# Kernel tuning notes

Hardware: AMD Instinct MI355X
Metric: run time of the kernel (lower is better)

Reference implementation:

```python
import jax, jax.numpy as jnp
import numpy as np
from jax.scipy.linalg import solve_triangular

B, N, C = 4, 1024, 1024
H, P = 16, 5
D = C // H
CHUNK = 64
EPS = 1e-8


def l2norm(x):
    return x * jax.lax.rsqrt(jnp.sum(x * x, -1, keepdims=True) + 1e-6)


def fir_conv(x, filt):
    # x: (B,N,H,D); filt: (H,D,K); causal depthwise FIR along sequence dim
    K = filt.shape[-1]
    n = x.shape[1]
    xp = jnp.pad(x, ((0, 0), (K - 1, 0), (0, 0), (0, 0)))
    out = jnp.zeros_like(x)
    for j in range(K):  # K in {3,7}: tiny fixed tap loop
        out = out + filt[:, :, j] * xp[:, j:j + n]
    return out


def cross_mix(x, mix):
    # residual low-magnitude cross-head mixing: (H,H) matrix applied over head axis
    return x + jnp.einsum('bnhd,hg->bngd', x, mix)


def delta_rule_chunkwise(q, k, v, beta, chunk=CHUNK):
    # q,k,v: (B,H,N,D); beta: (B,H,N). Chunkwise DeltaNet recurrence.
    b, h, n, d = q.shape
    q = l2norm(q) * (d ** -0.5)
    k = l2norm(k)
    v = v * beta[..., None]
    kb = k * beta[..., None]
    nc = n // chunk
    qc, kc, vc, kbc = (t.reshape(b, h, nc, chunk, d) for t in (q, k, v, kb))
    # (I + strict-lower(kb k^T))^{-1} applied to kb and v via triangular solve
    A = jnp.tril(jnp.einsum('bhgcd,bhged->bhgce', kbc, kc), -1)
    M = A + jnp.eye(chunk, dtype=q.dtype)
    w = solve_triangular(M, kbc, lower=True)   # (B,H,nc,chunk,D)
    u = solve_triangular(M, vc, lower=True)
    attn_loc = jnp.tril(jnp.einsum('bhgcd,bhged->bhgce', qc, kc))  # causal intra-chunk

    def step(S, xs):
        q_i, k_i, w_i, u_i, a_i = xs
        u_adj = u_i - jnp.einsum('bhcd,bhde->bhce', w_i, S)
        o_i = jnp.einsum('bhcd,bhde->bhce', q_i, S) + jnp.einsum('bhce,bhed->bhcd', a_i, u_adj)
        S = S + jnp.einsum('bhcd,bhce->bhde', k_i, u_adj)
        return S, o_i

    S0 = jnp.zeros((b, h, d, d), q.dtype)
    xs = tuple(jnp.moveaxis(t, 2, 0) for t in (qc, kc, w, u, attn_loc))
    S, o = jax.lax.scan(step, S0, xs)
    o = jnp.moveaxis(o, 0, 2).reshape(b, h, n, d)
    return o, S


def setup_inputs() -> dict:
    key = jax.random.key(0)
    ks = jax.random.split(key, 12)
    s = C ** -0.5
    inp = {}
    inp['x'] = jax.random.normal(ks[0], (B, N, C), jnp.float32)
    inp['W_qkv'] = jax.random.normal(ks[1], (C, 3 * C), jnp.float32) * s
    inp['W_id'] = jax.random.normal(ks[2], (C, C), jnp.float32) * s
    inp['W_gate'] = jax.random.normal(ks[3], (C, H), jnp.float32) * s
    inp['b_gate'] = jnp.full((H,), -1.5, jnp.float32)
    inp['id_static_logit'] = jnp.full((H,), float(np.log(0.2 / 0.8)), jnp.float32)
    dirac3 = jnp.zeros((H, D, 3), jnp.float32).at[:, :, -1].set(1.0)
    dirac7 = jnp.zeros((H, D, 7), jnp.float32).at[:, :, -1].set(1.0)
    inp['fir_s'] = dirac3 + 0.02 * jax.random.normal(ks[4], (H, D, 3), jnp.float32)
    inp['fir_l'] = dirac7 + 0.02 * jax.random.normal(ks[5], (H, D, 7), jnp.float32)
    inp['mix'] = 0.02 * jax.random.normal(ks[6], (H, H), jnp.float32)
    inp['W_prune'] = jax.random.normal(ks[7], (C, H * P), jnp.float32) * s
    inp['b_prune'] = jnp.zeros((H * P,), jnp.float32)
    inp['W_g1'] = jax.random.normal(ks[8], (C, C), jnp.float32) * s
    inp['b_g1'] = jnp.zeros((C,), jnp.float32)
    inp['W_g2'] = jax.random.normal(ks[9], (C, H * P), jnp.float32) * s
    inp['b_g2'] = jnp.zeros((H * P,), jnp.float32)
    inp['W_proj'] = jax.random.normal(ks[10], (C, C), jnp.float32) * s
    inp['b_proj'] = jnp.zeros((C,), jnp.float32)
    return inp


def reference(x, W_qkv, W_id, W_gate, b_gate, id_static_logit, fir_s, fir_l, mix,
              W_prune, b_prune, W_g1, b_g1, W_g2, b_g2, W_proj, b_proj):
    b, n, c = x.shape
    qkv = (x @ W_qkv).reshape(b, n, 3, H, D).transpose(2, 0, 3, 1, 4)  # (3,B,H,N,D)
    q, k, v = qkv[0], qkv[1], qkv[2]

    # gated identity path
    identity = (x @ W_id).reshape(b, n, H, D)
    dyn_gate = jax.nn.sigmoid(x @ W_gate + b_gate)            # (B,N,H)
    id_gate = dyn_gate * jax.nn.sigmoid(id_static_logit)      # static per-head gate
    identity = identity * id_gate[..., None]

    # delta-rule branch with linearly decaying beta
    beta = jnp.broadcast_to(jnp.linspace(1.0, 0.1, n, dtype=x.dtype)[None, None, :], (b, H, n))
    delta_out, _ = delta_rule_chunkwise(q, k, v, beta)
    delta_out = delta_out.transpose(0, 2, 1, 3)               # (B,N,H,D)

    # FIR branches on V with cross-head mixing
    v_hnd = v.transpose(0, 2, 1, 3)                            # (B,N,H,D)
    fs = cross_mix(fir_conv(v_hnd, fir_s), mix)
    fl = cross_mix(fir_conv(v_hnd, fir_l), mix)

    paths = jnp.stack([fs, fl, delta_out, v_hnd, identity], axis=3)  # (B,N,H,P,D)

    # progressive pruning prior
    prune_probs = jax.nn.softmax((x @ W_prune + b_prune).reshape(b, n, H, P), -1)
    ent1 = -jnp.mean(jnp.sum(prune_probs * jnp.log(prune_probs + EPS), -1))

    # context-adaptive gating fused with pruning prior
    h = jax.nn.gelu(x @ W_g1 + b_g1)
    gate_logits = (h @ W_g2 + b_g2).reshape(b, n, H, P)
    w_gate = jax.nn.softmax(gate_logits + jnp.log(prune_probs + EPS), -1)
    ent2 = -jnp.mean(jnp.sum(w_gate * jnp.log(w_gate + EPS), -1))

    ctx = jnp.einsum('bnhp,bnhpd->bnhd', w_gate, paths)
    out = ctx.reshape(b, n, c) @ W_proj + b_proj
    return out, ent1 + ent2
```

## Files before the change

### kernel.cpp

```cpp
#include <hip/hip_runtime.h>
#include <math.h>

#define B_ 4
#define N_ 1024
#define C_ 1024
#define H_ 16
#define D_ 64
#define P_ 5
#define BN_ (B_*N_)
#define TOK 8

typedef unsigned int u32;
typedef unsigned short u16;
typedef __attribute__((ext_vector_type(8))) short bf16x8;
typedef __attribute__((ext_vector_type(4))) float f32x4;

__device__ __forceinline__ float gelu_f(float x){
  float x3 = x*x*x;
  return 0.5f*x*(1.0f + tanhf(0.7978845608028654f*(x + 0.044715f*x3)));
}
__device__ __forceinline__ float sigmoid_f(float x){ return 1.0f/(1.0f+expf(-x)); }

__device__ __forceinline__ u16 f2bf(float f) {
  u32 u = __float_as_uint(f);
  u32 r = u + 0x7fffu + ((u >> 16) & 1u);
  return (u16)(r >> 16);
}
__device__ __forceinline__ float bf2f(u16 v){ return __uint_as_float(((u32)v) << 16); }

__device__ __forceinline__ void gload16(const void* g, void* l) {
  __builtin_amdgcn_global_load_lds((const __attribute__((address_space(1))) u32*)g,
                                   (__attribute__((address_space(3))) u32*)l, 16, 0, 0);
}

__device__ __forceinline__ void trans_block(const float* __restrict__ W,
    u16* __restrict__ Wt, int K, int Nn, int roff, int bxx, int byy,
    float (*t)[33], int tid) {
  const int c0 = bxx * 32, r0 = byy * 32;
  const int tx = tid & 31, ty = tid >> 5;
  #pragma unroll
  for (int i = 0; i < 4; ++i) {
    int r = ty + i * 8;
    t[r][tx] = (c0 + tx < Nn) ? W[(size_t)(r0 + r) * Nn + c0 + tx] : 0.f;
  }
  __syncthreads();
  #pragma unroll
  for (int i = 0; i < 4; ++i) {
    int r = ty + i * 8;
    if (c0 + r < Nn)
      Wt[(size_t)(roff + c0 + r) * K + r0 + tx] = f2bf(t[tx][r]);
  }
}

__global__ __launch_bounds__(256) void setup_k(const float* __restrict__ x,
    const float* __restrict__ W_qkv, const float* __restrict__ W_id,
    const float* __restrict__ W_g1, const float* __restrict__ W_proj,
    const float* __restrict__ W_gate, const float* __restrict__ W_prune,
    const float* __restrict__ W_g2, const float* __restrict__ bg,
    const float* __restrict__ bp, const float* __restrict__ bg2,
    u16* __restrict__ xb, u16* __restrict__ wcat, u16* __restrict__ wprojT,
    u16* __restrict__ catG2, float* __restrict__ cb1, float* __restrict__ cb2,
    float* __restrict__ entA) {
  __shared__ float t[32][33];
  int bid = blockIdx.x;
  const int tid = threadIdx.x;
  if (bid < 2048) {
    int i = bid * 256 + tid;
    const float4* p = (const float4*)x + (size_t)i * 2;
    float4 a = p[0], b = p[1];
    uint4 o;
    o.x = (u32)f2bf(a.x) | ((u32)f2bf(a.y) << 16);
    o.y = (u32)f2bf(a.z) | ((u32)f2bf(a.w) << 16);
    o.z = (u32)f2bf(b.x) | ((u32)f2bf(b.y) << 16);
    o.w = (u32)f2bf(b.z) | ((u32)f2bf(b.w) << 16);
    *(uint4*)(xb + (size_t)i * 8) = o;
    return;
  }
  bid -= 2048;
  if (bid < 3072) { trans_block(W_qkv, wcat, 1024, 3072, 0, bid % 96, bid / 96, t, tid); return; }
  bid -= 3072;
  if (bid < 1024) { trans_block(W_id, wcat, 1024, 1024, 3072, bid & 31, bid >> 5, t, tid); return; }
  bid -= 1024;
  if (bid < 1024) { trans_block(W_g1, wcat, 1024, 1024, 4096, bid & 31, bid >> 5, t, tid); return; }
  bid -= 1024;
  if (bid < 1024) { trans_block(W_proj, wprojT, 1024, 1024, 0, bid & 31, bid >> 5, t, tid); return; }
  bid -= 1024;
  if (bid < 32)  { trans_block(W_gate, wcat, 1024, 16, 5120, 0, bid, t, tid); return; }
  bid -= 32;
  if (bid < 96)  { trans_block(W_prune, wcat, 1024, 80, 5136, bid % 3, bid / 3, t, tid); return; }
  bid -= 96;
  if (bid < 96)  { trans_block(W_g2, catG2, 1024, 80, 0, bid % 3, bid / 3, t, tid); return; }
  bid -= 96;
  if (bid < 8) {
    int idx = (bid * 256 + tid) * 16;
    *(uint4*)(wcat + (size_t)5216 * 1024 + idx) = make_uint4(0, 0, 0, 0);
    *(uint4*)(wcat + (size_t)5216 * 1024 + idx + 8) = make_uint4(0, 0, 0, 0);
    return;
  }
  bid -= 8;
  if (bid < 12) {
    int idx = (bid * 256 + tid) * 16;
    *(uint4*)(catG2 + 80 * 1024 + idx) = make_uint4(0, 0, 0, 0);
    *(uint4*)(catG2 + 80 * 1024 + idx + 8) = make_uint4(0, 0, 0, 0);
    return;
  }
  if (tid < 128) cb1[tid] = (tid < 16) ? bg[tid] : (tid < 96 ? bp[tid - 16] : 0.f);
  else { int c = tid - 128; cb2[c] = (c < 80) ? bg2[c] : 0.f; }
  if (tid == 0) entA[0] = 0.f;
}

template<int ACT, int OBF, int NORM, int ENT>
__global__ __launch_bounds__(256) void gemm_mfma(const u16* __restrict__ A,
    const u16* __restrict__ Bt, const float* __restrict__ bias,
    float* __restrict__ Cout, int M, int Nn, int K, int Ns,
    const float* __restrict__ entSrc, float* __restrict__ entDst) {
  __shared__ __align__(16) u16 lA[3][128 * 32];
  __shared__ __align__(16) u16 lB[3][128 * 32];
  const int tid = threadIdx.x;
  const int lane = tid & 63, wid = tid >> 6;
  const int wr = wid >> 1, wc = wid & 1;
  const int r16 = lane & 15, kq = lane >> 4;
  const int row0 = blockIdx.y * 128, col0 = blockIdx.x * 128;
  const int c0 = wid * 2;
  const int srow = lane >> 2;
  const int skoff = (((lane & 3) ^ ((srow >> 1) & 3)) << 3);
  const int rsw = ((r16 >> 1) & 3);
  const int T = K >> 5;

  if (ENT && blockIdx.x == 0 && blockIdx.y == 0 && tid == 0)
    entDst[0] = entSrc[0] * (1.0f / 65536.0f);

  #define STAGE_T(buf, tk) { \
    const int k0_ = (tk) << 5; \
    _Pragma("unroll") \
    for (int s = 0; s < 2; ++s) { \
      int c = c0 + s; \
      int rt = c * 16 + srow; \
      gload16(A  + (size_t)(row0 + rt) * K + k0_ + skoff, &lA[buf][c * 512]); \
      gload16(Bt + (size_t)(col0 + rt) * K + k0_ + skoff, &lB[buf][c * 512]); \
    } }

  f32x4 acc[4][4] = {};
  STAGE_T(0, 0);
  if (T > 1) STAGE_T(1, 1);

  for (int t = 0; t < T; ++t) {
    if (t < T - 1) asm volatile("s_waitcnt vmcnt(4)" ::: "memory");
    else           asm volatile("s_waitcnt vmcnt(0)" ::: "memory");
    __builtin_amdgcn_s_barrier();
    asm volatile("" ::: "memory");
    if (t + 2 < T) { const int bnx = (t + 2) % 3; STAGE_T(bnx, t + 2); }
    const int bc = t % 3;
    const int ko = ((kq ^ rsw) << 3);
    bf16x8 af[4], bfv[4];
    #pragma unroll
    for (int m = 0; m < 4; ++m)
      af[m] = *(const bf16x8*)&lA[bc][(wr * 64 + m * 16 + r16) * 32 + ko];
    #pragma unroll
    for (int n = 0; n < 4; ++n)
      bfv[n] = *(const bf16x8*)&lB[bc][(wc * 64 + n * 16 + r16) * 32 + ko];
    #pragma unroll
    for (int m = 0; m < 4; ++m)
      #pragma unroll
      for (int n = 0; n < 4; ++n)
        acc[m][n] = __builtin_amdgcn_mfma_f32_16x16x32_bf16(af[m], bfv[n], acc[m][n], 0, 0, 0);
  }
  #undef STAGE_T

  if (NORM) {
    const int hb = (col0 + wc * 64) >> 6;
    if (hb < 32) {
      float sc[4][4];
      #pragma unroll
      for (int m = 0; m < 4; ++m)
        #pragma unroll
        for (int r = 0; r < 4; ++r) {
          float s = 0.f;
          #pragma unroll
          for (int n = 0; n < 4; ++n) s = fmaf(acc[m][n][r], acc[m][n][r], s);
          s += __shfl_xor(s, 1); s += __shfl_xor(s, 2);
          s += __shfl_xor(s, 4); s += __shfl_xor(s, 8);
          float tsc = rsqrtf(s + 1e-6f);
          sc[m][r] = (hb < 16) ? tsc * 0.125f : tsc;
        }
      #pragma unroll
      for (int m = 0; m < 4; ++m)
        #pragma unroll
        for (int n = 0; n < 4; ++n)
          #pragma unroll
          for (int r = 0; r < 4; ++r) acc[m][n][r] *= sc[m][r];
    }
  }

  #pragma unroll
  for (int n = 0; n < 4; ++n) {
    int col = col0 + wc * 64 + n * 16 + r16;
    if (col >= Ns) continue;
    float bs = bias ? bias[col] : 0.0f;
    #pragma unroll
    for (int m = 0; m < 4; ++m) {
      int rowb = row0 + wr * 64 + m * 16 + kq * 4;
      #pragma unroll
      for (int r = 0; r < 4; ++r) {
        float v = acc[m][n][r] + bs;
        if (ACT == 1) v = gelu_f(v);
        if (OBF) ((u16*)Cout)[(size_t)(rowb + r) * Ns + col] = f2bf(v);
        else     Cout[(size_t)(rowb + r) * Ns + col] = v;
      }
    }
  }
}

__global__ __launch_bounds__(256) void gemm_g1gp(const u16* __restrict__ A,
    const u16* __restrict__ Bt, const float* __restrict__ b_g1,
    const float* __restrict__ cb1, u16* __restrict__ hb16,
    float* __restrict__ gp) {
  __shared__ __align__(16) u16 lA[3][128 * 32];
  __shared__ __align__(16) u16 lB[3][128 * 32];
  const int tid = threadIdx.x;
  const int lane = tid & 63, wid = tid >> 6;
  const int wr = wid >> 1, wc = wid & 1;
  const int r16 = lane & 15, kq = lane >> 4;
  const int row0 = blockIdx.y * 128, col0 = blockIdx.x * 128;
  const int K = 1024, T = 32;
  const int c0 = wid * 2;
  const int srow = lane >> 2;
  const int skoff = (((lane & 3) ^ ((srow >> 1) & 3)) << 3);
  const int rsw = ((r16 >> 1) & 3);

  #define STAGE_T(buf, tk) { \
    const int k0_ = (tk) << 5; \
    _Pragma("unroll") \
    for (int s = 0; s < 2; ++s) { \
      int c = c0 + s; \
      int rt = c * 16 + srow; \
      gload16(A  + (size_t)(row0 + rt) * K + k0_ + skoff, &lA[buf][c * 512]); \
      gload16(Bt + (size_t)(col0 + rt) * K + k0_ + skoff, &lB[buf][c * 512]); \
    } }

  f32x4 acc[4][4] = {};
  STAGE_T(0, 0);
  STAGE_T(1, 1);
  for (int t = 0; t < T; ++t) {
    if (t < T - 1) asm volatile("s_waitcnt vmcnt(4)" ::: "memory");
    else           asm volatile("s_waitcnt vmcnt(0)" ::: "memory");
    __builtin_amdgcn_s_barrier();
    asm volatile("" ::: "memory");
    if (t + 2 < T) { const int bnx = (t + 2) % 3; STAGE_T(bnx, t + 2); }
    const int bc = t % 3;
    const int ko = ((kq ^ rsw) << 3);
    bf16x8 af[4], bfv[4];
    #pragma unroll
    for (int m = 0; m < 4; ++m)
      af[m] = *(const bf16x8*)&lA[bc][(wr * 64 + m * 16 + r16) * 32 + ko];
    #pragma unroll
    for (int n = 0; n < 4; ++n)
      bfv[n] = *(const bf16x8*)&lB[bc][(wc * 64 + n * 16 + r16) * 32 + ko];
    #pragma unroll
    for (int m = 0; m < 4; ++m)
      #pragma unroll
      for (int n = 0; n < 4; ++n)
        acc[m][n] = __builtin_amdgcn_mfma_f32_16x16x32_bf16(af[m], bfv[n], acc[m][n], 0, 0, 0);
  }
  #undef STAGE_T

  const int hb = (col0 + wc * 64) >> 6;
  #pragma unroll
  for (int n = 0; n < 4; ++n) {
    const int col = col0 + wc * 64 + n * 16 + r16;
    if (hb < 16) {
      const float bs = b_g1[col];
      #pragma unroll
      for (int m = 0; m < 4; ++m) {
        int rowb = row0 + wr * 64 + m * 16 + kq * 4;
        #pragma unroll
        for (int r = 0; r < 4; ++r)
          hb16[(size_t)(rowb + r) * 1024 + col] = f2bf(gelu_f(acc[m][n][r] + bs));
      }
    } else {
      const int c2 = col - 1024;
      if (c2 < 96) {
        const float bs = cb1[c2];
        #pragma unroll
        for (int m = 0; m < 4; ++m) {
          int rowb = row0 + wr * 64 + m * 16 + kq * 4;
          #pragma unroll
          for (int r = 0; r < 4; ++r)
            gp[(size_t)(rowb + r) * 96 + c2] = acc[m][n][r] + bs;
        }
      }
    }
  }
}

__global__ __launch_bounds__(256) void delta_prep(const u16* __restrict__ qkvi,
    u16* __restrict__ tb) {
  const int bx = blockIdx.x;
  const int bh = bx >> 4, g = bx & 15;
  const int b = bh >> 4, h = bh & 15;
  const int n0 = g * 64;
  const int tid = threadIdx.x;
  __shared__ __align__(16) u16 sKb[64][72];
  __shared__ __align__(16) float sMT[64][68];
  __shared__ float sBeta[64];

  if (tid < 64) sBeta[tid] = 1.0f - 0.9f * (float)(n0 + tid) / 1023.0f;

  const int fr = tid >> 2, fe0 = (tid & 3) * 16;
  const size_t krow = ((size_t)b * N_ + n0 + fr) * 4096 + 1024 + h * 64 + fe0;
  *(uint4*)&sKb[fr][fe0]     = *(const uint4*)(qkvi + krow);
  *(uint4*)&sKb[fr][fe0 + 8] = *(const uint4*)(qkvi + krow + 8);
  __syncthreads();

  {
    const int lane = tid & 63, wv = tid >> 6;
    const int l15 = lane & 15, l4 = lane >> 4;
    bf16x8 ka0 = *(const bf16x8*)&sKb[16*wv + l15][l4*8];
    bf16x8 ka1 = *(const bf16x8*)&sKb[16*wv + l15][32 + l4*8];
    #pragma unroll
    for (int ct = 0; ct < 4; ++ct) {
      bf16x8 kc0 = *(const bf16x8*)&sKb[ct*16 + l15][l4*8];
      bf16x8 kc1 = *(const bf16x8*)&sKb[ct*16 + l15][32 + l4*8];
      f32x4 m = {};
      m = __builtin_amdgcn_mfma_f32_16x16x32_bf16(ka0, kc0, m, 0, 0, 0);
      m = __builtin_amdgcn_mfma_f32_16x16x32_bf16(ka1, kc1, m, 0, 0, 0);
      const int c = ct*16 + l15, rbase = 16*wv + l4*4;
      float4 o;
      o.x = (rbase+0 > c) ? sBeta[rbase+0] * m[0] : 0.f;
      o.y = (rbase+1 > c) ? sBeta[rbase+1] * m[1] : 0.f;
      o.z = (rbase+2 > c) ? sBeta[rbase+2] * m[2] : 0.f;
      o.w = (rbase+3 > c) ? sBeta[rbase+3] * m[3] : 0.f;
      *(float4*)&sMT[c][rbase] = o;
    }
  }
  __syncthreads();

  if (tid < 64) {
    const int c = tid;
    float a[64];
    #pragma unroll
    for (int i = 0; i < 64; ++i) a[i] = (i == c) ? 1.f : 0.f;
    #pragma unroll
    for (int ib = 0; ib < 4; ++ib) {
      #pragma unroll
      for (int i2 = 0; i2 < 16; ++i2) {
        const int i = ib * 16 + i2;
        const float wi = a[i];
        #pragma unroll
        for (int j4 = ib * 4; j4 < 16; ++j4) {
          const float4 m = *(const float4*)&sMT[i][j4 * 4];
          a[j4*4+0] = fmaf(-m.x, wi, a[j4*4+0]);
          a[j4*4+1] = fmaf(-m.y, wi, a[j4*4+1]);
          a[j4*4+2] = fmaf(-m.z, wi, a[j4*4+2]);
          a[j4*4+3] = fmaf(-m.w, wi, a[j4*4+3]);
        }
      }
    }
    const float bc = sBeta[c];
    const size_t obase = (size_t)bx * 4096;
    #pragma unroll
    for (int i = 0; i < 64; ++i) tb[obase + i * 64 + c] = f2bf(a[i] * bc);
  }
}

__global__ __launch_bounds__(256, 1) void delta_fused(const u16* __restrict__ tb,
    const u16* __restrict__ qkvi, u16* __restrict__ dOutb) {
  const int bh = blockIdx.x >> 1, h2 = blockIdx.x & 1;
  const int b = bh >> 4, h = bh & 15;
  const int dvo = h2 * 32;
  const int tid = threadIdx.x;
  const int lane = tid & 63, wv = tid >> 6;
  const int l15 = lane & 15, l4 = lane >> 4;
  const int fr = tid >> 2, fe0 = (tid & 3) * 16;
  const int fe2 = (tid & 3) * 8;

  __shared__ __align__(16) u16 sK [64][72];
  __shared__ __align__(16) u16 sKT[64][72];
  __shared__ __align__(16) u16 sT [64][72];
  __shared__ __align__(16) u16 sQ [64][72];
  __shared__ __align__(16) u16 sV [64][40];
  __shared__ __align__(16) u16 sSt[32][72];
  __shared__ __align__(16) u16 sYt[32][72];
  __shared__ __align__(16) u16 sUt[32][72];
  __shared__ __align__(16) u16 sA [64][72];

  f32x4 Sacc[2] = {};

  uint4 pk0, pk1, pt0, pt1, pq0, pq1, pv0;
  {
    const size_t bs = (size_t)(bh * 16) * 4096;
    const size_t rowq = ((size_t)(b * 1024 + fr)) * 4096 + h * 64 + fe0;
    const size_t rowv = ((size_t)(b * 1024 + fr)) * 4096 + 2048 + h * 64 + dvo + fe2;
    pq0 = *(const uint4*)(qkvi + rowq);        pq1 = *(const uint4*)(qkvi + rowq + 8);
    pk0 = *(const uint4*)(qkvi + rowq + 1024); pk1 = *(const uint4*)(qkvi + rowq + 1024 + 8);
    pv0 = *(const uint4*)(qkvi + rowv);
    pt0 = *(const uint4*)(tb + bs + tid*16);   pt1 = *(const uint4*)(tb + bs + tid*16 + 8);
  }

  for (int g = 0; g < 16; ++g) {
    __syncthreads();
    *(uint4*)&sK[fr][fe0] = pk0; *(uint4*)&sK[fr][fe0+8] = pk1;
    *(uint4*)&sT[fr][fe0] = pt0; *(uint4*)&sT[fr][fe0+8] = pt1;
    *(uint4*)&sQ[fr][fe0] = pq0; *(uint4*)&sQ[fr][fe0+8] = pq1;
    *(uint4*)&sV[fr][fe2] = pv0;
    {
      u32 kk[8] = {pk0.x, pk0.y, pk0.z, pk0.w, pk1.x, pk1.y, pk1.z, pk1.w};
      #pragma unroll
      for (int i = 0; i < 8; ++i) {
        sKT[fe0 + 2*i][fr]     = (u16)kk[i];
        sKT[fe0 + 2*i + 1][fr] = (u16)(kk[i] >> 16);
      }
    }
    #pragma unroll
    for (int dt = 0; dt < 2; ++dt) {
      u32 lo = (u32)f2bf(Sacc[dt][0]) | ((u32)f2bf(Sacc[dt][1]) << 16);
      u32 hi = (u32)f2bf(Sacc[dt][2]) | ((u32)f2bf(Sacc[dt][3]) << 16);
      *(u32*)&sSt[dt*16 + l15][16*wv + l4*4]     = lo;
      *(u32*)&sSt[dt*16 + l15][16*wv + l4*4 + 2] = hi;
    }
    __syncthreads();
    if (g < 15) {
      const size_t bs = (size_t)(bh * 16 + g + 1) * 4096;
      const size_t rowq = ((size_t)(b * 1024 + (g + 1) * 64 + fr)) * 4096 + h * 64 + fe0;
      const size_t rowv = ((size_t)(b * 1024 + (g + 1) * 64 + fr)) * 4096 + 2048 + h * 64 + dvo + fe2;
      pq0 = *(const uint4*)(qkvi + rowq);        pq1 = *(const uint4*)(qkvi + rowq + 8);
      pk0 = *(const uint4*)(qkvi + rowq + 1024); pk1 = *(const uint4*)(qkvi + rowq + 1024 + 8);
      pv0 = *(const uint4*)(qkvi + rowv);
      pt0 = *(const uint4*)(tb + bs + tid*16);   pt1 = *(const uint4*)(tb + bs + tid*16 + 8);
    }
    bf16x8 qf0 = *(const bf16x8*)&sQ[16*wv + l15][l4*8];
    bf16x8 qf1 = *(const bf16x8*)&sQ[16*wv + l15][32 + l4*8];
    bf16x8 kr0 = *(const bf16x8*)&sK[16*wv + l15][l4*8];
    bf16x8 kr1 = *(const bf16x8*)&sK[16*wv + l15][32 + l4*8];
    f32x4 aacc[4] = {}, yacc[2] = {}, oacc[2] = {};
    #pragma unroll
    for (int ct = 0; ct < 4; ++ct) {
      bf16x8 kc0 = *(const bf16x8*)&sK[ct*16 + l15][l4*8];
      bf16x8 kc1 = *(const bf16x8*)&sK[ct*16 + l15][32 + l4*8];
      aacc[ct] = __builtin_amdgcn_mfma_f32_16x16x32_bf16(qf0, kc0, aacc[ct], 0, 0, 0);
      aacc[ct] = __builtin_amdgcn_mfma_f32_16x16x32_bf16(qf1, kc1, aacc[ct], 0, 0, 0);
    }
    #pragma unroll
    for (int dt = 0; dt < 2; ++dt) {
      bf16x8 s0 = *(const bf16x8*)&sSt[dt*16 + l15][l4*8];
      bf16x8 s1 = *(const bf16x8*)&sSt[dt*16 + l15][32 + l4*8];
      yacc[dt] = __builtin_amdgcn_mfma_f32_16x16x32_bf16(kr0, s0, yacc[dt], 0, 0, 0);
      yacc[dt] = __builtin_amdgcn_mfma_f32_16x16x32_bf16(kr1, s1, yacc[dt], 0, 0, 0);
      oacc[dt] = __builtin_amdgcn_mfma_f32_16x16x32_bf16(qf0, s0, oacc[dt], 0, 0, 0);
      oacc[dt] = __builtin_amdgcn_mfma_f32_16x16x32_bf16(qf1, s1, oacc[dt], 0, 0, 0);
    }
    #pragma unroll
    for (int dt = 0; dt < 2; ++dt) {
      float y0 = bf2f(sV[16*wv + l4*4 + 0][dt*16 + l15]) - yacc[dt][0];
      float y1 = bf2f(sV[16*wv + l4*4 + 1][dt*16 + l15]) - yacc[dt][1];
      float y2 = bf2f(sV[16*wv + l4*4 + 2][dt*16 + l15]) - yacc[dt][2];
      float y3 = bf2f(sV[16*wv + l4*4 + 3][dt*16 + l15]) - yacc[dt][3];
      u32 lo = (u32)f2bf(y0) | ((u32)f2bf(y1) << 16);
      u32 hi = (u32)f2bf(y2) | ((u32)f2bf(y3) << 16);
      *(u32*)&sYt[dt*16 + l15][16*wv + l4*4]     = lo;
      *(u32*)&sYt[dt*16 + l15][16*wv + l4*4 + 2] = hi;
    }
    #pragma unroll
    for (int ct = 0; ct < 4; ++ct)
      #pragma unroll
      for (int j = 0; j < 4; ++j) {
        int r = 16*wv + l4*4 + j, c = ct*16 + l15;
        sA[r][c] = f2bf((r >= c) ? aacc[ct][j] : 0.f);
      }
    __syncthreads();
    bf16x8 tf0 = *(const bf16x8*)&sT[16*wv + l15][l4*8];
    bf16x8 tf1 = *(const bf16x8*)&sT[16*wv + l15][32 + l4*8];
    f32x4 uacc[2] = {};
    #pragma unroll
    for (int dt = 0; dt < 2; ++dt) {
      bf16x8 y0 = *(const bf16x8*)&sYt[dt*16 + l15][l4*8];
      bf16x8 y1 = *(const bf16x8*)&sYt[dt*16 + l15][32 + l4*8];
      uacc[dt] = __builtin_amdgcn_mfma_f32_16x16x32_bf16(tf0, y0, uacc[dt], 0, 0, 0);
      uacc[dt] = __builtin_amdgcn_mfma_f32_16x16x32_bf16(tf1, y1, uacc[dt], 0, 0, 0);
    }
    #pragma unroll
    for (int dt = 0; dt < 2; ++dt) {
      u32 lo = (u32)f2bf(uacc[dt][0]) | ((u32)f2bf(uacc[dt][1]) << 16);
      u32 hi = (u32)f2bf(uacc[dt][2]) | ((u32)f2bf(uacc[dt][3]) << 16);
      *(u32*)&sUt[dt*16 + l15][16*wv + l4*4]     = lo;
      *(u32*)&sUt[dt*16 + l15][16*wv + l4*4 + 2] = hi;
    }
    __syncthreads();
    bf16x8 af0 = *(const bf16x8*)&sA[16*wv + l15][l4*8];
    bf16x8 af1 = *(const bf16x8*)&sA[16*wv + l15][32 + l4*8];
    bf16x8 kt0 = *(const bf16x8*)&sKT[16*wv + l15][l4*8];
    bf16x8 kt1 = *(const bf16x8*)&sKT[16*wv + l15][32 + l4*8];
    #pragma unroll
    for (int dt = 0; dt < 2; ++dt) {
      bf16x8 u0 = *(const bf16x8*)&sUt[dt*16 + l15][l4*8];
      bf16x8 u1 = *(const bf16x8*)&sUt[dt*16 + l15][32 + l4*8];
      oacc[dt] = __builtin_amdgcn_mfma_f32_16x16x32_bf16(af0, u0, oacc[dt], 0, 0, 0);
      oacc[dt] = __builtin_amdgcn_mfma_f32_16x16x32_bf16(af1, u1, oacc[dt], 0, 0, 0);
      Sacc[dt] = __builtin_amdgcn_mfma_f32_16x16x32_bf16(kt0, u0, Sacc[dt], 0, 0, 0);
      Sacc[dt] = __builtin_amdgcn_mfma_f32_16x16x32_bf16(kt1, u1, Sacc[dt], 0, 0, 0);
    }
    #pragma unroll
    for (int dt = 0; dt < 2; ++dt)
      #pragma unroll
      for (int j = 0; j < 4; ++j) {
        int r = 16*wv + l4*4 + j;
        dOutb[((size_t)(b * 1024 + g * 64 + r)) * 1024 + h * 64 + dvo + dt*16 + l15] = f2bf(oacc[dt][j]);
      }
  }
}

__global__ __launch_bounds__(256) void paths2(const u16* __restrict__ qkvi,
    const u16* __restrict__ dOutb, const float* __restrict__ gp,
    const float* __restrict__ g2L, const float* __restrict__ fir_s,
    const float* __restrict__ fir_l, const float* __restrict__ mix,
    const float* __restrict__ idlog, u16* __restrict__ ctxb,
    float* __restrict__ entAcc) {
  const int bid = ((blockIdx.x & 7) << 6) | (blockIdx.x >> 3);
  const int b = bid >> 7, n0 = (bid & 127) * TOK;
  const int tid = threadIdx.x;
  __shared__ u16 sV[TOK + 6][1024];
  __shared__ u16 sFS[TOK][1024], sFL[TOK][1024];
  __shared__ float sMix[256];
  __shared__ float sWg[TOK][16][5];
  __shared__ float sIdg[TOK][16];
  __shared__ float sEnt[128];
  sMix[tid] = mix[tid];

  #pragma unroll
  for (int i = 0; i < 7; ++i) {
    int r = i * 2 + (tid >> 7);
    int t = n0 - 6 + r;
    int col = (tid & 127) * 8;
    uint4 v = make_uint4(0, 0, 0, 0);
    if (t >= 0)
      v = *(const uint4*)(qkvi + ((size_t)b * 1024 + t) * 4096 + 2048 + col);
    *(uint4*)&sV[r][col] = v;
  }

  if (tid < 128) {
    const int tok = tid >> 4, hh = tid & 15;
    const size_t bn = (size_t)b * 1024 + n0 + tok;
    float pl[5], lp[5];
    #pragma unroll
    for (int p = 0; p < 5; ++p) pl[p] = gp[bn * 96 + 16 + hh * 5 + p];
    float mx = pl[0];
    #pragma unroll
    for (int p = 1; p < 5; ++p) mx = fmaxf(mx, pl[p]);
    float s = 0.f;
    #pragma unroll
    for (int p = 0; p < 5; ++p) { pl[p] = expf(pl[p] - mx); s += pl[p]; }
    float inv = 1.f / s, e1 = 0.f;
    #pragma unroll
    for (int p = 0; p < 5; ++p) {
      float prob = pl[p] * inv;
      lp[p] = logf(prob + 1e-8f);
      e1 -= prob * lp[p];
    }
    float gl[5];
    #pragma unroll
    for (int p = 0; p < 5; ++p) gl[p] = g2L[bn * 80 + hh * 5 + p] + lp[p];
    float mx2 = gl[0];
    #pragma unroll
    for (int p = 1; p < 5; ++p) mx2 = fmaxf(mx2, gl[p]);
    float s2 = 0.f;
    #pragma unroll
    for (int p = 0; p < 5; ++p) { gl[p] = expf(gl[p] - mx2); s2 += gl[p]; }
    float inv2 = 1.f / s2, e2 = 0.f;
    #pragma unroll
    for (int p = 0; p < 5; ++p) {
      float w = gl[p] * inv2;
      sWg[tok][hh][p] = w;
      e2 -= w * logf(w + 1e-8f);
    }
    sEnt[tid] = e1 + e2;
    sIdg[tok][hh] = sigmoid_f(gp[bn * 96 + hh]) * sigmoid_f(idlog[hh]);
  }
  __syncthreads();

  #pragma unroll
  for (int i = 0; i < 4; ++i) {
    const int idx = tid + i * 256;
    float fl7[7], fs3[3];
    #pragma unroll
    for (int j = 0; j < 7; ++j) fl7[j] = fir_l[(size_t)idx * 7 + j];
    #pragma unroll
    for (int j = 0; j < 3; ++j) fs3[j] = fir_s[(size_t)idx * 3 + j];
    #pragma unroll
    for (int tok = 0; tok < TOK; ++tok) {
      float accs = 0.f, accl = 0.f;
      #pragma unroll
      for (int j = 0; j < 7; ++j) {
        float vv = bf2f(sV[tok + j][idx]);
        accl = fmaf(fl7[j], vv, accl);
        if (j >= 4) accs = fmaf(fs3[j - 4], vv, accs);
      }
      sFS[tok][idx] = f2bf(accs);
      sFL[tok][idx] = f2bf(accl);
    }
  }
  __syncthreads();

  #pragma unroll
  for (int i = 0; i < 4; ++i) {
    const int idx = tid + i * 256;
    const int gg = idx >> 6, d = idx & 63;
    #pragma unroll
    for (int tok = 0; tok < TOK; ++tok) {
      float as = bf2f(sFS[tok][idx]), al = bf2f(sFL[tok][idx]);
      #pragma unroll
      for (int hh = 0; hh < 16; ++hh) {
        float m = sMix[hh * 16 + gg];
        as = fmaf(bf2f(sFS[tok][hh * 64 + d]), m, as);
        al = fmaf(bf2f(sFL[tok][hh * 64 + d]), m, al);
      }
      const size_t bn = (size_t)b * 1024 + n0 + tok;
      float w0 = sWg[tok][gg][0], w1 = sWg[tok][gg][1], w2 = sWg[tok][gg][2];
      float w3 = sWg[tok][gg][3], w4 = sWg[tok][gg][4];
      float dv = bf2f(dOutb[bn * 1024 + idx]);
      float vv = bf2f(sV[tok + 6][idx]);
      float iv = bf2f(qkvi[bn * 4096 + 3072 + idx]) * sIdg[tok][gg];
      ctxb[bn * 1024 + idx] = f2bf(w0*as + w1*al + w2*dv + w3*vv + w4*iv);
    }
  }
  if (tid == 0) {
    float s = 0.f;
    #pragma unroll
    for (int i = 0; i < 128; ++i) s += sEnt[i];
    atomicAdd(entAcc, s);
  }
}

extern "C" void kernel_launch(void* const* d_in, const int* in_sizes, int n_in,
                              void* d_out, int out_size, void* d_ws, size_t ws_size,
                              hipStream_t stream) {
  (void)in_sizes; (void)n_in; (void)out_size; (void)ws_size;
  const float* x       = (const float*)d_in[0];
  const float* W_qkv   = (const float*)d_in[1];
  const float* W_id    = (const float*)d_in[2];
  const float* W_gate  = (const float*)d_in[3];
  const float* b_gate  = (const float*)d_in[4];
  const float* idlog   = (const float*)d_in[5];
  const float* fir_s   = (const float*)d_in[6];
  const float* fir_l   = (const float*)d_in[7];
  const float* mix     = (const float*)d_in[8];
  const float* W_prune = (const float*)d_in[9];
  const float* b_prune = (const float*)d_in[10];
  const float* W_g1    = (const float*)d_in[11];
  const float* b_g1    = (const float*)d_in[12];
  const float* W_g2    = (const float*)d_in[13];
  const float* b_g2    = (const float*)d_in[14];
  const float* W_proj  = (const float*)d_in[15];
  const float* b_proj  = (const float*)d_in[16];
  float* out = (float*)d_out;

  float* ws    = (float*)d_ws;
  float* qkviF = ws;
  float* gp    = ws + 8388608;
  float* g2l   = gp + 393216;
  float* kbF   = g2l + 327680;
  float* wcatF = kbF + 2097152;
  float* catG2F= wcatF + 2686976;
  float* dOb   = catG2F + 65536;
  float* entA  = dOb + 2097152;
  float* cb1   = entA + 8;
  float* cb2   = cb1 + 128;
  float* wprF  = cb2 + 128;

  u16* qkvi   = (u16*)qkviF;
  u16* wcat   = (u16*)wcatF;
  u16* tb16   = (u16*)wcatF;
  u16* catG2  = (u16*)catG2F;
  u16* dOutb  = (u16*)dOb;
  u16* wprojT = (u16*)wprF;
  u16* xb     = (u16*)kbF;
  u16* hb16   = (u16*)dOb;
  u16* ctxb   = (u16*)kbF;

  setup_k<<<8437, 256, 0, stream>>>(x, W_qkv, W_id, W_g1, W_proj, W_gate,
                                    W_prune, W_g2, b_gate, b_prune, b_g2,
                                    xb, wcat, wprojT, catG2, cb1, cb2, entA);

  gemm_mfma<0,1,1,0><<<dim3(32, 32), 256, 0, stream>>>(xb, wcat, nullptr,
      (float*)qkvi, BN_, 4096, 1024, 4096, nullptr, nullptr);

  gemm_g1gp<<<dim3(9, 32), 256, 0, stream>>>(xb, wcat + (size_t)4096 * 1024,
                                             b_g1, cb1, hb16, gp);

  gemm_mfma<0,0,0,0><<<dim3(1, 32), 256, 0, stream>>>(hb16, catG2, cb2, g2l,
      BN_, 128, 1024, 80, nullptr, nullptr);

  delta_prep<<<1024, 256, 0, stream>>>(qkvi, tb16);
  delta_fused<<<128, 256, 0, stream>>>(tb16, qkvi, dOutb);

  paths2<<<512, 256, 0, stream>>>(qkvi, dOutb, gp, g2l,
                                  fir_s, fir_l, mix, idlog, ctxb, entA);

  gemm_mfma<0,0,0,1><<<dim3(8, 32), 256, 0, stream>>>(ctxb, wprojT, b_proj, out,
      BN_, 1024, 1024, 1024, entA, out + 4194304);
}
```

Before: 243.7 us.

## Use 256x128 tiles with 512-thread blocks for the QKV and output GEMMs

Adds a gemm_mfma2 kernel that uses 8 waves and a 256x128 output tile. The A tile is twice as tall, so each B tile loaded into LDS is shared across more rows. It replaces the 128x128 kernel for the large QKV projection and the final output projection, halving the grid's row dimension. LDS grows to about 72KB per block, which can reduce how many blocks fit per CU and lowers the block count. The small G2 GEMM keeps the old kernel, now stripped of its NORM and ENT paths.

```diff
diff --git a/kernel.cpp b/kernel.cpp
--- a/kernel.cpp
+++ b/kernel.cpp
@@ -109,11 +109,113 @@
   if (tid == 0) entA[0] = 0.f;
 }
 
-template<int ACT, int OBF, int NORM, int ENT>
-__global__ __launch_bounds__(256) void gemm_mfma(const u16* __restrict__ A,
+template<int OBF, int NORM, int ENT>
+__global__ __launch_bounds__(512, 4) void gemm_mfma2(const u16* __restrict__ A,
     const u16* __restrict__ Bt, const float* __restrict__ bias,
     float* __restrict__ Cout, int M, int Nn, int K, int Ns,
     const float* __restrict__ entSrc, float* __restrict__ entDst) {
+  __shared__ __align__(16) u16 lA[3][256 * 32];
+  __shared__ __align__(16) u16 lB[3][128 * 32];
+  const int tid = threadIdx.x;
+  const int lane = tid & 63, wid = tid >> 6;
+  const int wr = wid >> 1, wc = wid & 1;
+  const int r16 = lane & 15, kq = lane >> 4;
+  const int row0 = blockIdx.y * 256, col0 = blockIdx.x * 128;
+  const int srow = lane >> 2;
+  const int skoff = (((lane & 3) ^ ((srow >> 1) & 3)) << 3);
+  const int rsw = ((r16 >> 1) & 3);
+  const int T = K >> 5;
+
+  if (ENT && blockIdx.x == 0 && blockIdx.y == 0 && tid == 0)
+    entDst[0] = entSrc[0] * (1.0f / 65536.0f);
+
+  #define STAGE2(buf, tk) { \
+    const int k0_ = (tk) << 5; \
+    _Pragma("unroll") \
+    for (int s = 0; s < 2; ++s) { \
+      int c = wid * 2 + s; \
+      int rt = c * 16 + srow; \
+      gload16(A + (size_t)(row0 + rt) * K + k0_ + skoff, &lA[buf][c * 512]); \
+    } \
+    { \
+      int rtB = wid * 16 + srow; \
+      gload16(Bt + (size_t)(col0 + rtB) * K + k0_ + skoff, &lB[buf][wid * 512]); \
+    } }
+
+  f32x4 acc[4][4] = {};
+  STAGE2(0, 0);
+  STAGE2(1, 1);
+
+  for (int t = 0; t < T; ++t) {
+    if (t < T - 1) asm volatile("s_waitcnt vmcnt(3)" ::: "memory");
+    else           asm volatile("s_waitcnt vmcnt(0)" ::: "memory");
+    __builtin_amdgcn_s_barrier();
+    asm volatile("" ::: "memory");
+    if (t + 2 < T) { const int bnx = (t + 2) % 3; STAGE2(bnx, t + 2); }
+    const int bc = t % 3;
+    const int ko = ((kq ^ rsw) << 3);
+    bf16x8 af[4], bfv[4];
+    #pragma unroll
+    for (int m = 0; m < 4; ++m)
+      af[m] = *(const bf16x8*)&lA[bc][(wr * 64 + m * 16 + r16) * 32 + ko];
+    #pragma unroll
+    for (int n = 0; n < 4; ++n)
+      bfv[n] = *(const bf16x8*)&lB[bc][(wc * 64 + n * 16 + r16) * 32 + ko];
+    #pragma unroll
+    for (int m = 0; m < 4; ++m)
+      #pragma unroll
+      for (int n = 0; n < 4; ++n)
+        acc[m][n] = __builtin_amdgcn_mfma_f32_16x16x32_bf16(af[m], bfv[n], acc[m][n], 0, 0, 0);
+  }
+  #undef STAGE2
+
+  if (NORM) {
+    const int hb = (col0 + wc * 64) >> 6;
+    if (hb < 32) {
+      float sc[4][4];
+      #pragma unroll
+      for (int m = 0; m < 4; ++m)
+        #pragma unroll
+        for (int r = 0; r < 4; ++r) {
+          float s = 0.f;
+          #pragma unroll
+          for (int n = 0; n < 4; ++n) s = fmaf(acc[m][n][r], acc[m][n][r], s);
+          s += __shfl_xor(s, 1); s += __shfl_xor(s, 2);
+          s += __shfl_xor(s, 4); s += __shfl_xor(s, 8);
+          float tsc = rsqrtf(s + 1e-6f);
+          sc[m][r] = (hb < 16) ? tsc * 0.125f : tsc;
+        }
+      #pragma unroll
+      for (int m = 0; m < 4; ++m)
+        #pragma unroll
+        for (int n = 0; n < 4; ++n)
+          #pragma unroll
+          for (int r = 0; r < 4; ++r) acc[m][n][r] *= sc[m][r];
+    }
+  }
+
+  #pragma unroll
+  for (int n = 0; n < 4; ++n) {
+    int col = col0 + wc * 64 + n * 16 + r16;
+    if (col >= Ns) continue;
+    float bs = bias ? bias[col] : 0.0f;
+    #pragma unroll
+    for (int m = 0; m < 4; ++m) {
+      int rowb = row0 + wr * 64 + m * 16 + kq * 4;
+      #pragma unroll
+      for (int r = 0; r < 4; ++r) {
+        float v = acc[m][n][r] + bs;
+        if (OBF) ((u16*)Cout)[(size_t)(rowb + r) * Ns + col] = f2bf(v);
+        else     Cout[(size_t)(rowb + r) * Ns + col] = v;
+      }
+    }
+  }
+}
+
+template<int ACT, int OBF>
+__global__ __launch_bounds__(256) void gemm_mfma(const u16* __restrict__ A,
+    const u16* __restrict__ Bt, const float* __restrict__ bias,
+    float* __restrict__ Cout, int M, int Nn, int K, int Ns) {
   __shared__ __align__(16) u16 lA[3][128 * 32];
   __shared__ __align__(16) u16 lB[3][128 * 32];
   const int tid = threadIdx.x;
@@ -127,9 +229,6 @@
   const int rsw = ((r16 >> 1) & 3);
   const int T = K >> 5;
 
-  if (ENT && blockIdx.x == 0 && blockIdx.y == 0 && tid == 0)
-    entDst[0] = entSrc[0] * (1.0f / 65536.0f);
-
   #define STAGE_T(buf, tk) { \
     const int k0_ = (tk) << 5; \
     _Pragma("unroll") \
@@ -166,31 +265,6 @@
         acc[m][n] = __builtin_amdgcn_mfma_f32_16x16x32_bf16(af[m], bfv[n], acc[m][n], 0, 0, 0);
   }
   #undef STAGE_T
-
-  if (NORM) {
-    const int hb = (col0 + wc * 64) >> 6;
-    if (hb < 32) {
-      float sc[4][4];
-      #pragma unroll
-      for (int m = 0; m < 4; ++m)
-        #pragma unroll
-        for (int r = 0; r < 4; ++r) {
-          float s = 0.f;
-          #pragma unroll
-          for (int n = 0; n < 4; ++n) s = fmaf(acc[m][n][r], acc[m][n][r], s);
-          s += __shfl_xor(s, 1); s += __shfl_xor(s, 2);
-          s += __shfl_xor(s, 4); s += __shfl_xor(s, 8);
-          float tsc = rsqrtf(s + 1e-6f);
-          sc[m][r] = (hb < 16) ? tsc * 0.125f : tsc;
-        }
-      #pragma unroll
-      for (int m = 0; m < 4; ++m)
-        #pragma unroll
-        for (int n = 0; n < 4; ++n)
-          #pragma unroll
-          for (int r = 0; r < 4; ++r) acc[m][n][r] *= sc[m][r];
-    }
-  }
 
   #pragma unroll
   for (int n = 0; n < 4; ++n) {
@@ -680,14 +754,14 @@
                                     W_prune, W_g2, b_gate, b_prune, b_g2,
                                     xb, wcat, wprojT, catG2, cb1, cb2, entA);
 
-  gemm_mfma<0,1,1,0><<<dim3(32, 32), 256, 0, stream>>>(xb, wcat, nullptr,
+  gemm_mfma2<1,1,0><<<dim3(32, 16), 512, 0, stream>>>(xb, wcat, nullptr,
       (float*)qkvi, BN_, 4096, 1024, 4096, nullptr, nullptr);
 
   gemm_g1gp<<<dim3(9, 32), 256, 0, stream>>>(xb, wcat + (size_t)4096 * 1024,
                                              b_g1, cb1, hb16, gp);
 
-  gemm_mfma<0,0,0,0><<<dim3(1, 32), 256, 0, stream>>>(hb16, catG2, cb2, g2l,
-      BN_, 128, 1024, 80, nullptr, nullptr);
+  gemm_mfma<0,0><<<dim3(1, 32), 256, 0, stream>>>(hb16, catG2, cb2, g2l,
+      BN_, 128, 1024, 80);
 
   delta_prep<<<1024, 256, 0, stream>>>(qkvi, tb16);
   delta_fused<<<128, 256, 0, stream>>>(tb16, qkvi, dOutb);
@@ -695,6 +769,6 @@
   paths2<<<512, 256, 0, stream>>>(qkvi, dOutb, gp, g2l,
                                   fir_s, fir_l, mix, idlog, ctxb, entA);
 
-  gemm_mfma<0,0,0,1><<<dim3(8, 32), 256, 0, stream>>>(ctxb, wprojT, b_proj, out,
+  gemm_mfma2<0,0,1><<<dim3(8, 16), 512, 0, stream>>>(ctxb, wprojT, b_proj, out,
       BN_, 1024, 1024, 1024, entA, out + 4194304);
 }
```

After: 233.4 us. 4.2% less time.
